# Kernel tuning notes

Hardware: AMD Instinct MI355X
Metric: run time of the kernel (lower is better)

Reference implementation:

```python
import jax, jax.numpy as jnp
import numpy as np

L = 2048           # lattice side
R = 2.777          # public-goods multiplier r
GAMMA = 0.8
ETA = 0.8
K_FERMI = 0.5      # fermi temperature used in fermiUpdate


def _plus_sum(x):
    """3x3 plus-kernel conv with circular (wrap) padding == self + 4 rolled neighbors."""
    return (x
            + jnp.roll(x, 1, 0) + jnp.roll(x, -1, 0)
            + jnp.roll(x, 1, 1) + jnp.roll(x, -1, 1))


def setup_inputs() -> dict:
    key = jax.random.key(0)
    k1, k2, k3, k4, k5 = jax.random.split(key, 5)
    return {
        "type_t_minus": jax.random.randint(k1, (L, L), 0, 2, dtype=jnp.int32),
        "type_t": jax.random.randint(k2, (L, L), 0, 2, dtype=jnp.int32),
        "Q_tensor": jax.random.normal(k3, (L * L, 2, 2), dtype=jnp.float32),
        "learning_direction": jax.random.randint(k4, (L, L), 0, 4, dtype=jnp.int32),
        "learning_probabilities": jax.random.uniform(k5, (L, L), dtype=jnp.float32),
    }


def reference(type_t_minus, type_t, Q_tensor, learning_direction, learning_probabilities):
    N = L * L
    # ---- calculation_value: per-cell payoff from the 5 overlapping PGG games ----
    c = (type_t == 1).astype(jnp.float32)   # cooperator mask
    d = (type_t == 0).astype(jnp.float32)   # defector mask
    coop_num = _plus_sum(c)                  # cooperators in own 5-cell group
    base = coop_num * (R / 5.0)
    profit = _plus_sum(base - 1.0) * c + _plus_sum(base) * d   # [L, L]

    # ---- updateQMatrix: Q[C, A, B] <- (1-eta)*Q[C,A,B] + eta*(profit + gamma*max_b Q[C,B,b]) ----
    A = type_t_minus.reshape(-1)             # previous action, [N]
    B = type_t.reshape(-1)                   # current action,  [N]
    Qb = jnp.take_along_axis(Q_tensor, B[:, None, None], axis=1)[:, 0, :]  # Q[C, B, :] -> [N, 2]
    max_values = Qb.max(axis=1)              # [N]
    flatQ = Q_tensor.reshape(N, 4)
    idx = A * 2 + B                          # flattened (A, B) index
    old = jnp.take_along_axis(flatQ, idx[:, None], axis=1)[:, 0]
    upd = (1.0 - ETA) * old + ETA * (profit.reshape(-1) + GAMMA * max_values)
    Q_new = flatQ.at[jnp.arange(N), idx].set(upd).reshape(N, 2, 2)

    # ---- fermiUpdate: gather just-updated Q[C,A,B] (== upd), compare with 4 neighbors ----
    pm = upd.reshape(L, L)                   # fermi profit matrix

    def W(shift, axis):
        return 1.0 / (1.0 + jnp.exp((pm - jnp.roll(pm, shift, axis)) / K_FERMI))

    Ws = jnp.stack([W(1, 1), W(-1, 1), W(1, 0), W(-1, 0)])        # left,right,up,down [4,L,L]
    nb = jnp.stack([jnp.roll(type_t, 1, 1), jnp.roll(type_t, -1, 1),
                    jnp.roll(type_t, 1, 0), jnp.roll(type_t, -1, 0)])
    W_sel = jnp.take_along_axis(Ws, learning_direction[None], axis=0)[0]
    nb_sel = jnp.take_along_axis(nb, learning_direction[None], axis=0)[0]
    type_t1 = jnp.where(learning_probabilities <= W_sel, nb_sel, type_t)  # [L, L] int32

    return (Q_new, type_t1, profit)
```

## Files before the change

### kernel.cpp

```cpp
#include <hip/hip_runtime.h>


#define LSIDE 2048
#define LMASK 2047
#define LSHIFT 11
#define NCELL (LSIDE * LSIDE)

#define TROWS 7
#define TCOLS 264

__global__ __launch_bounds__(256) void spgg_fused(
    const int* __restrict__ tmin,
    const int* __restrict__ tt,
    const float* __restrict__ Q,
    const int* __restrict__ ldir,
    const float* __restrict__ lp,
    float* __restrict__ Qn,
    float* __restrict__ prof,
    float* __restrict__ t1out)
{
    __shared__ int tile[TROWS][TCOLS];

    const int t   = threadIdx.x;
    const int blk = blockIdx.x;
    const int i   = blk >> 3;
    const int j0  = (blk & 7) << 8;

    for (int k = t; k < TROWS * (TCOLS / 4); k += 256) {
        int r = k / (TCOLS / 4);
        int m = k - r * (TCOLS / 4);
        int row_g = (i + r - 3) & LMASK;
        int col_g = (j0 - 4 + (m << 2)) & LMASK;
        int4 v = *(const int4*)&tt[(row_g << LSHIFT) + col_g];
        *(int4*)&tile[r][m << 2] = v;
    }
    __syncthreads();

    const float KB        = 0.5554f;
    const float ETA       = 0.8f;
    const float ONE_M_ETA = 0.2f;
    const float GAMMA     = 0.8f;

#define M(r, c) (tile[r][c] == 1)

    auto profit_at = [&](int r, int c) -> float {
        int m_cc = M(r, c);
        int cn_c = m_cc + M(r-1, c) + M(r+1, c) + M(r, c-1) + M(r, c+1);
        int cn_u = M(r-1, c) + M(r-2, c) + m_cc + M(r-1, c-1) + M(r-1, c+1);
        int cn_d = M(r+1, c) + m_cc + M(r+2, c) + M(r+1, c-1) + M(r+1, c+1);
        int cn_l = M(r, c-1) + M(r-1, c-1) + M(r+1, c-1) + M(r, c-2) + m_cc;
        int cn_r = M(r, c+1) + M(r-1, c+1) + M(r+1, c+1) + m_cc + M(r, c+2);
        float b_c = __fmul_rn((float)cn_c, KB);
        float b_u = __fmul_rn((float)cn_u, KB);
        float b_d = __fmul_rn((float)cn_d, KB);
        float b_l = __fmul_rn((float)cn_l, KB);
        float b_r = __fmul_rn((float)cn_r, KB);
        float s0 = __fadd_rn(__fadd_rn(__fadd_rn(__fadd_rn(b_c, b_u), b_d), b_l), b_r);
        float s1 = __fadd_rn(__fadd_rn(__fadd_rn(__fadd_rn(
                       __fsub_rn(b_c, 1.0f), __fsub_rn(b_u, 1.0f)),
                       __fsub_rn(b_d, 1.0f)), __fsub_rn(b_l, 1.0f)),
                       __fsub_rn(b_r, 1.0f));
        return m_cc ? s1 : s0;
    };

    auto upd_of = [&](float profit, float4 qr, int A, int B) -> float {
        float q0 = (B == 0) ? qr.x : qr.z;
        float q1 = (B == 0) ? qr.y : qr.w;
        float mx = fmaxf(q0, q1);
        int k = A * 2 + B;
        float old = (k == 0) ? qr.x : ((k == 1) ? qr.y : ((k == 2) ? qr.z : qr.w));
        float t0 = __fmul_rn(GAMMA, mx);
        float t1 = __fadd_rn(profit, t0);
        float t2 = __fmul_rn(ETA, t1);
        float t3 = __fmul_rn(ONE_M_ETA, old);
        return __fadd_rn(t3, t2);
    };

    const int j   = j0 + t;
    const int idx = (i << LSHIFT) + j;
    const int lr  = 3, lc = t + 4;

    float p_own = profit_at(lr, lc);
    float4 qr   = ((const float4*)Q)[idx];
    int B = tile[lr][lc];
    int A = tmin[idx];
    float upd = upd_of(p_own, qr, A, B);

    int k = A * 2 + B;
    float4 qo;
    qo.x = (k == 0) ? upd : qr.x;
    qo.y = (k == 1) ? upd : qr.y;
    qo.z = (k == 2) ? upd : qr.z;
    qo.w = (k == 3) ? upd : qr.w;
    ((float4*)Qn)[idx] = qo;
    prof[idx] = p_own;

    int dir = ldir[idx];
    int di = (dir == 3) - (dir == 2);
    int dj = (dir == 1) - (dir == 0);
    int ni = (i + di) & LMASK;
    int nj = (j + dj) & LMASK;
    int nidx = (ni << LSHIFT) + nj;

    float p_nb  = profit_at(lr + di, lc + dj);
    float4 qn4  = ((const float4*)Q)[nidx];
    int Bn = tile[lr + di][lc + dj];
    int An = tmin[nidx];
    float upd_nb = upd_of(p_nb, qn4, An, Bn);

    float e1 = __fsub_rn(upd, upd_nb);
    float e2 = __fmul_rn(e1, 2.0f);
    float ex = (float)exp((double)e2);
    float W  = __fdiv_rn(1.0f, __fadd_rn(1.0f, ex));
    float pv = lp[idx];
    int sel = (pv <= W) ? Bn : B;
    t1out[idx] = (float)sel;
#undef M
}

extern "C" void kernel_launch(void* const* d_in, const int* in_sizes, int n_in,
                              void* d_out, int out_size, void* d_ws, size_t ws_size,
                              hipStream_t stream) {
    const int*   type_t_minus = (const int*)d_in[0];
    const int*   type_t       = (const int*)d_in[1];
    const float* Q_tensor     = (const float*)d_in[2];
    const int*   ldir         = (const int*)d_in[3];
    const float* lprob        = (const float*)d_in[4];

    float* out   = (float*)d_out;
    float* Qn    = out;
    float* t1out = out + (size_t)4 * NCELL;
    float* prof  = out + (size_t)5 * NCELL;

    const int threads = 256;
    const int blocks  = NCELL / threads;
    spgg_fused<<<blocks, threads, 0, stream>>>(type_t_minus, type_t, Q_tensor,
                                               ldir, lprob, Qn, prof, t1out);
}
```

Before: 216.3 us.

## Precompute group payoff bases in shared tile and hoist global loads before sync

Adds a second shared-memory tile that holds the per-cell cooperator-count base value (count times r/5) for a 5x260 region. Each cell's profit then becomes a 5-point stencil read from that tile instead of recounting the 25-cell neighbourhood. The per-cell global loads (direction, probability, Q row, previous action, and the neighbour's Q/action) are issued before the first barrier so their latency overlaps the tile fill. The cost is an extra barrier and more shared memory and live registers per block. It relies on the type values being exactly 0/1, since the tile entries are summed directly.

```diff
diff --git a/kernel.cpp b/kernel.cpp
--- a/kernel.cpp
+++ b/kernel.cpp
@@ -8,6 +8,8 @@
 
 #define TROWS 7
 #define TCOLS 264
+#define BROWS 5
+#define BCOLS 260
 
 __global__ __launch_bounds__(256) void spgg_fused(
     const int* __restrict__ tmin,
@@ -19,12 +21,20 @@
     float* __restrict__ prof,
     float* __restrict__ t1out)
 {
-    __shared__ int tile[TROWS][TCOLS];
+    __shared__ int   tile[TROWS][TCOLS];
+    __shared__ float btile[BROWS][BCOLS];
 
     const int t   = threadIdx.x;
     const int blk = blockIdx.x;
     const int i   = blk >> 3;
     const int j0  = (blk & 7) << 8;
+    const int j   = j0 + t;
+    const int idx = (i << LSHIFT) + j;
+
+    const int    dir = ldir[idx];
+    const float  pv  = lp[idx];
+    const float4 qr  = ((const float4*)Q)[idx];
+    const int    A   = tmin[idx];
 
     for (int k = t; k < TROWS * (TCOLS / 4); k += 256) {
         int r = k / (TCOLS / 4);
@@ -34,6 +44,15 @@
         int4 v = *(const int4*)&tt[(row_g << LSHIFT) + col_g];
         *(int4*)&tile[r][m << 2] = v;
     }
+
+    const int di = (dir == 3) - (dir == 2);
+    const int dj = (dir == 1) - (dir == 0);
+    const int ni = (i + di) & LMASK;
+    const int nj = (j + dj) & LMASK;
+    const int nidx = (ni << LSHIFT) + nj;
+    const float4 qn4 = ((const float4*)Q)[nidx];
+    const int    An  = tmin[nidx];
+
     __syncthreads();
 
     const float KB        = 0.5554f;
@@ -41,34 +60,41 @@
     const float ONE_M_ETA = 0.2f;
     const float GAMMA     = 0.8f;
 
-#define M(r, c) (tile[r][c] == 1)
+    auto bval = [&](int tr, int tc) -> float {
+        int cn = tile[tr][tc] + tile[tr-1][tc] + tile[tr+1][tc]
+               + tile[tr][tc-1] + tile[tr][tc+1];
+        return __fmul_rn((float)cn, KB);
+    };
+    #pragma unroll
+    for (int r = 0; r < BROWS; ++r)
+        btile[r][t] = bval(r + 1, t + 2);
+    if (t < BCOLS - 256) {
+        #pragma unroll
+        for (int r = 0; r < BROWS; ++r)
+            btile[r][256 + t] = bval(r + 1, 258 + t);
+    }
+    __syncthreads();
 
-    auto profit_at = [&](int r, int c) -> float {
-        int m_cc = M(r, c);
-        int cn_c = m_cc + M(r-1, c) + M(r+1, c) + M(r, c-1) + M(r, c+1);
-        int cn_u = M(r-1, c) + M(r-2, c) + m_cc + M(r-1, c-1) + M(r-1, c+1);
-        int cn_d = M(r+1, c) + m_cc + M(r+2, c) + M(r+1, c-1) + M(r+1, c+1);
-        int cn_l = M(r, c-1) + M(r-1, c-1) + M(r+1, c-1) + M(r, c-2) + m_cc;
-        int cn_r = M(r, c+1) + M(r-1, c+1) + M(r+1, c+1) + m_cc + M(r, c+2);
-        float b_c = __fmul_rn((float)cn_c, KB);
-        float b_u = __fmul_rn((float)cn_u, KB);
-        float b_d = __fmul_rn((float)cn_d, KB);
-        float b_l = __fmul_rn((float)cn_l, KB);
-        float b_r = __fmul_rn((float)cn_r, KB);
+    auto profit_from_b = [&](int r, int c, int coop) -> float {
+        float b_c = btile[r][c];
+        float b_u = btile[r-1][c];
+        float b_d = btile[r+1][c];
+        float b_l = btile[r][c-1];
+        float b_r = btile[r][c+1];
         float s0 = __fadd_rn(__fadd_rn(__fadd_rn(__fadd_rn(b_c, b_u), b_d), b_l), b_r);
         float s1 = __fadd_rn(__fadd_rn(__fadd_rn(__fadd_rn(
                        __fsub_rn(b_c, 1.0f), __fsub_rn(b_u, 1.0f)),
                        __fsub_rn(b_d, 1.0f)), __fsub_rn(b_l, 1.0f)),
                        __fsub_rn(b_r, 1.0f));
-        return m_cc ? s1 : s0;
+        return coop ? s1 : s0;
     };
 
-    auto upd_of = [&](float profit, float4 qr, int A, int B) -> float {
-        float q0 = (B == 0) ? qr.x : qr.z;
-        float q1 = (B == 0) ? qr.y : qr.w;
+    auto upd_of = [&](float profit, float4 q4, int Ai, int Bi) -> float {
+        float q0 = (Bi == 0) ? q4.x : q4.z;
+        float q1 = (Bi == 0) ? q4.y : q4.w;
         float mx = fmaxf(q0, q1);
-        int k = A * 2 + B;
-        float old = (k == 0) ? qr.x : ((k == 1) ? qr.y : ((k == 2) ? qr.z : qr.w));
+        int k = Ai * 2 + Bi;
+        float old = (k == 0) ? q4.x : ((k == 1) ? q4.y : ((k == 2) ? q4.z : q4.w));
         float t0 = __fmul_rn(GAMMA, mx);
         float t1 = __fadd_rn(profit, t0);
         float t2 = __fmul_rn(ETA, t1);
@@ -76,15 +102,9 @@
         return __fadd_rn(t3, t2);
     };
 
-    const int j   = j0 + t;
-    const int idx = (i << LSHIFT) + j;
-    const int lr  = 3, lc = t + 4;
-
-    float p_own = profit_at(lr, lc);
-    float4 qr   = ((const float4*)Q)[idx];
-    int B = tile[lr][lc];
-    int A = tmin[idx];
-    float upd = upd_of(p_own, qr, A, B);
+    const int B     = tile[3][t + 4];
+    float p_own = profit_from_b(2, t + 2, B);
+    float upd   = upd_of(p_own, qr, A, B);
 
     int k = A * 2 + B;
     float4 qo;
@@ -95,27 +115,16 @@
     ((float4*)Qn)[idx] = qo;
     prof[idx] = p_own;
 
-    int dir = ldir[idx];
-    int di = (dir == 3) - (dir == 2);
-    int dj = (dir == 1) - (dir == 0);
-    int ni = (i + di) & LMASK;
-    int nj = (j + dj) & LMASK;
-    int nidx = (ni << LSHIFT) + nj;
-
-    float p_nb  = profit_at(lr + di, lc + dj);
-    float4 qn4  = ((const float4*)Q)[nidx];
-    int Bn = tile[lr + di][lc + dj];
-    int An = tmin[nidx];
+    const int Bn = tile[3 + di][t + 4 + dj];
+    float p_nb   = profit_from_b(2 + di, t + 2 + dj, Bn);
     float upd_nb = upd_of(p_nb, qn4, An, Bn);
 
     float e1 = __fsub_rn(upd, upd_nb);
     float e2 = __fmul_rn(e1, 2.0f);
     float ex = (float)exp((double)e2);
     float W  = __fdiv_rn(1.0f, __fadd_rn(1.0f, ex));
-    float pv = lp[idx];
     int sel = (pv <= W) ? Bn : B;
     t1out[idx] = (float)sel;
-#undef M
 }
 
 extern "C" void kernel_launch(void* const* d_in, const int* in_sizes, int n_in,
```

Measured after the change: 220.5 us. No clear change (+1.9%).
